# Kernel tuning notes

Hardware: AMD Instinct MI355X
Metric: run time of the kernel (lower is better)

The kernel has to match this reference:

```python
import jax, jax.numpy as jnp
import numpy as np
from jax import lax

# dims
B = 1024          # batch
C_IN = 8          # board feature planes
HW = 8            # board side
FN = 16           # filter_num
SEN, INT, OUT = 1024, 2048, 1024
TOT = SEN + INT + OUT            # 4096
CNN_OUT = sum((HW - k + 1) ** 2 for k in range(1, 9)) * FN  # 204*FN = 3264
NUM_OUT = 1968
LORA_R = 64
LORA_SCALE = 128.0 / LORA_R      # alpha / rank = 2.0
TIMESTEPS = 5
DENSITY = 0.3


def setup_inputs() -> dict:
    key = jax.random.key(0)
    ks = jax.random.split(key, 20)
    inp = {"x": jax.random.normal(ks[0], (B, HW, HW, C_IN), dtype=jnp.float32)}
    # conv bank: kernels 1..8, OIHW layout
    for i, k in enumerate(range(1, 9)):
        inp[f"conv_w{k}"] = jax.random.normal(ks[1 + i], (FN, C_IN, k, k), dtype=jnp.float32) * (1.0 / np.sqrt(C_IN * k * k))
    inp["conv_b"] = jnp.zeros((8, FN), dtype=jnp.float32)
    # recurrent weight with sparsity pattern (mask = W != 0, as in register_buffer('sparsity_mask', W_init != 0))
    Wd = jax.random.normal(ks[9], (TOT, TOT), dtype=jnp.float32) * 0.02
    mask = (jax.random.uniform(ks[10], (TOT, TOT)) < DENSITY).astype(jnp.float32)
    inp["W"] = Wd * mask
    inp["lora_A"] = jax.random.normal(ks[11], (TOT, LORA_R), dtype=jnp.float32) * 0.02
    inp["lora_B"] = jax.random.normal(ks[12], (LORA_R, TOT), dtype=jnp.float32) * 0.02
    inp["ip_w"] = jax.random.normal(ks[13], (CNN_OUT, SEN), dtype=jnp.float32) * (1.0 / np.sqrt(CNN_OUT))
    inp["ip_b"] = jnp.zeros((SEN,), dtype=jnp.float32)
    inp["out_w"] = jax.random.normal(ks[14], (OUT, NUM_OUT), dtype=jnp.float32) * (1.0 / np.sqrt(OUT))
    inp["out_b"] = jnp.zeros((NUM_OUT,), dtype=jnp.float32)
    return inp


def _forward(x, conv_w1, conv_w2, conv_w3, conv_w4, conv_w5, conv_w6, conv_w7, conv_w8,
             conv_b, W, lora_A, lora_B, ip_w, ip_b, out_w, out_b):
    xn = jnp.transpose(x, (0, 3, 1, 2))  # NHWC -> NCHW, as x.permute(0,3,1,2)
    feats = []
    for i, cw in enumerate([conv_w1, conv_w2, conv_w3, conv_w4, conv_w5, conv_w6, conv_w7, conv_w8]):
        y = lax.conv_general_dilated(xn, cw, (1, 1), 'VALID',
                                     dimension_numbers=('NCHW', 'OIHW', 'NCHW'))
        y = jax.nn.relu(y + conv_b[i][None, :, None, None])  # use_relu=True
        feats.append(y.reshape(y.shape[0], -1))
    feat = jnp.concatenate(feats, axis=1)  # [B, CNN_OUT]

    # effective W with LoRA + sparsity mask
    mask = (W != 0).astype(W.dtype)
    W_eff = (W + (lora_A @ lora_B) * LORA_SCALE) * mask

    E = feat @ ip_w + ip_b                           # input_proj (no dropout: drop_out=False)
    E_pad = jnp.pad(E, ((0, 0), (0, TOT - SEN)))     # E feeds only the sensory block

    # The nine block matmuls S@Wss + I@Wrs + O@Wos etc. equal slices of state @ W_eff.
    state = jnp.zeros((x.shape[0], TOT), dtype=W.dtype)
    for t in range(TIMESTEPS):
        nxt = state @ W_eff
        if t == 0:
            nxt = nxt + E_pad
        nxt = state + nxt          # use_residual=True
        state = jax.nn.relu(nxt)

    O_state = state[:, SEN + INT:]
    return O_state @ out_w + out_b


def reference(x, conv_w1, conv_w2, conv_w3, conv_w4, conv_w5, conv_w6, conv_w7, conv_w8,
              conv_b, W, lora_A, lora_B, ip_w, ip_b, out_w, out_b):
    return _forward(x, conv_w1, conv_w2, conv_w3, conv_w4, conv_w5, conv_w6, conv_w7, conv_w8,
                    conv_b, W, lora_A, lora_B, ip_w, ip_b, out_w, out_b)
```

## Files before the change

kernel.cpp:

```cpp
#include <hip/hip_runtime.h>
#include <stdint.h>

typedef unsigned short u16;
typedef __attribute__((ext_vector_type(8))) short bf16x8;
typedef __attribute__((ext_vector_type(4))) float f32x4;

__device__ __forceinline__ u16 f2bf(float f) {
  union { float f; uint32_t u; } v; v.f = f;
  uint32_t u = v.u;
  return (u16)((u + 0x7fffu + ((u >> 16) & 1u)) >> 16);
}

__device__ __forceinline__ void gl_lds16(const void* g, void* l) {
  __builtin_amdgcn_global_load_lds(
      (const __attribute__((address_space(1))) uint32_t*)g,
      (__attribute__((address_space(3))) uint32_t*)l, 16, 0, 0);
}

__constant__ int c_off[9] = {0, 1024, 1808, 2384, 2784, 3040, 3184, 3248, 3264};

__global__ __launch_bounds__(256)
void prep_all(const float* __restrict__ x, u16* __restrict__ Xb,
              const float* __restrict__ lA, u16* __restrict__ lAb,
              const float* __restrict__ ip_w, u16* __restrict__ ip_wt,
              const float* __restrict__ out_w, u16* __restrict__ out_wt,
              const float* __restrict__ lB, u16* __restrict__ lBt,
              const float* w1, const float* w2, const float* w3, const float* w4,
              const float* w5, const float* w6, const float* w7, const float* w8,
              const float* __restrict__ cb,
              u16* __restrict__ Wct, float* __restrict__ bias_c) {
  __shared__ float tile[64][65];
  int b = blockIdx.x;
  const int t = threadIdx.x;
  if (b < 512) {
    const int i = b * 256 + t;
    const float4 v = ((const float4*)x)[i];
    ((ushort4*)Xb)[i] = make_ushort4(f2bf(v.x), f2bf(v.y), f2bf(v.z), f2bf(v.w));
    return;
  }
  b -= 512;
  if (b < 256) {
    const int i = b * 256 + t;
    const float4 v = ((const float4*)lA)[i];
    ((ushort4*)lAb)[i] = make_ushort4(f2bf(v.x), f2bf(v.y), f2bf(v.z), f2bf(v.w));
    return;
  }
  b -= 256;
  if (b < 1392) {
    const float* src; u16* dst; int R, C, bx, by;
    if (b < 816)        { src = ip_w;  dst = ip_wt;  R = 3264; C = 1024; bx = b % 16; by = b / 16; }
    else if (b < 1328)  { b -= 816;  src = out_w; dst = out_wt; R = 1024; C = 1968; bx = b % 32; by = b / 32; }
    else                { b -= 1328; src = lB;    dst = lBt;    R = 64;   C = 4096; bx = b;      by = 0; }
    const int rb = by << 6, cbs = bx << 6;
    for (int i = 0; i < 16; ++i) {
      const int idx = t + (i << 8);
      const int r = idx >> 6, c = idx & 63;
      float v = 0.f;
      if (cbs + c < C) v = src[(size_t)(rb + r) * C + cbs + c];
      tile[r][c] = v;
    }
    __syncthreads();
    for (int i = 0; i < 16; ++i) {
      const int idx = t + (i << 8);
      const int c = idx >> 6, r = idx & 63;
      dst[(size_t)(cbs + c) * R + rb + r] = f2bf(tile[r][c]);
    }
    return;
  }
  const int o = b - 1392;
  u16* row = Wct + (size_t)o * 512;
  if (t < 128) *(ushort4*)(row + (t << 2)) = make_ushort4(0, 0, 0, 0);
  if (o >= 3264) {
    if (t == 0) bias_c[o] = 0.f;
    return;
  }
  __syncthreads();
  const float* ws[8] = {w1, w2, w3, w4, w5, w6, w7, w8};
  int kidx = 0;
  while (o >= c_off[kidx + 1]) ++kidx;
  const int ks = kidx + 1;
  const int s  = 8 - kidx;
  const int r  = o - c_off[kidx];
  const int f   = r / (s * s);
  const int rem = r - f * s * s;
  const int oi  = rem / s;
  const int oj  = rem - oi * s;
  const float* w = ws[kidx] + (size_t)f * 8 * ks * ks;
  const int ne = 8 * ks * ks;
  for (int e = t; e < ne; e += 256) {
    const int c  = e / (ks * ks);
    const int er = e - c * ks * ks;
    const int di = er / ks;
    const int dj = er - di * ks;
    row[((oi + di) * 8 + (oj + dj)) * 8 + c] = f2bf(w[(c * ks + di) * ks + dj]);
  }
  if (t == 0) bias_c[o] = cb[kidx * 16 + f];
}

__global__ __launch_bounds__(256)
void weff2(const float* __restrict__ W, const u16* __restrict__ lBt,
           const u16* __restrict__ lAb, u16* __restrict__ Wt) {
  __shared__ __align__(16) u16 As_[64 * 64];
  __shared__ __align__(16) u16 Bs_[64 * 64];
  __shared__ __align__(16) float Wl[64 * 64];
  __shared__ u16 Ct[64 * 68];
  const int t = threadIdx.x;
  const int w = t >> 6, lane = t & 63;
  const int nb = blockIdx.x << 6, kb = blockIdx.y << 6;
  const int m0 = (w & 1) << 5, n0 = (w >> 1) << 5;
  const int lr = lane & 15, lq = lane >> 4;

  for (int i = 0; i < 2; ++i) {
    const int c   = (w << 7) + (i << 6) + lane;
    const int row = c >> 3;
    const int kg  = (c & 7) ^ (row & 7);
    gl_lds16(lBt + (size_t)(nb + row) * 64 + (kg << 3), (char*)As_ + c * 16);
    gl_lds16(lAb + (size_t)(kb + row) * 64 + (kg << 3), (char*)Bs_ + c * 16);
  }
  for (int i = 0; i < 4; ++i) {
    const int c   = (w << 8) + (i << 6) + lane;
    const int row = c >> 4;
    const int cc  = (c & 15) ^ (row & 15);
    gl_lds16(W + (size_t)(kb + row) * 4096 + nb + (cc << 2), (char*)Wl + c * 16);
  }
  __syncthreads();

  f32x4 acc[2][2] = {};
  for (int kk = 0; kk < 2; ++kk) {
    const int kg = (kk << 2) + lq;
    const int sw = (kg ^ (lr & 7)) << 3;
    bf16x8 af[2], bf[2];
    for (int i = 0; i < 2; ++i)
      af[i] = *(const bf16x8*)&As_[(m0 + (i << 4) + lr) * 64 + sw];
    for (int j = 0; j < 2; ++j)
      bf[j] = *(const bf16x8*)&Bs_[(n0 + (j << 4) + lr) * 64 + sw];
    for (int i = 0; i < 2; ++i)
      for (int j = 0; j < 2; ++j)
        acc[i][j] = __builtin_amdgcn_mfma_f32_16x16x32_bf16(af[i], bf[j], acc[i][j], 0, 0, 0);
  }

  for (int i = 0; i < 2; ++i) {
    for (int j = 0; j < 2; ++j) {
      const int cg  = n0 + (j << 4) + lr;
      const int rg0 = m0 + (i << 4) + (lq << 2);
      const int ch  = (rg0 >> 2) ^ (cg & 15);
      const float4 wv4 = *(const float4*)&Wl[cg * 64 + (ch << 2)];
      const float wv[4] = {wv4.x, wv4.y, wv4.z, wv4.w};
      for (int r = 0; r < 4; ++r)
        Ct[(rg0 + r) * 68 + cg] =
            (wv[r] != 0.f) ? f2bf(wv[r] + 2.0f * acc[i][j][r]) : (u16)0;
    }
  }
  __syncthreads();

  const int row = t >> 2, kp = (t & 3) << 4;
  u16* dst = Wt + (size_t)(nb + row) * 4096 + kb + kp;
  const u16* src = &Ct[row * 68 + kp];
  for (int i = 0; i < 4; ++i)
    *(ushort4*)(dst + (i << 2)) = *(const ushort4*)(src + (i << 2));
}

template<int EPI>
__global__ __launch_bounds__(256)
void gemm128(const u16* __restrict__ A, int lda,
             const u16* __restrict__ Bt, int ldb, int K,
             const float* __restrict__ bias,
             const float* __restrict__ st_in, int st_ld,
             float* __restrict__ outf, int outf_ld,
             u16* __restrict__ outb, int outb_ld, int nvalid) {
  __shared__ __align__(16) u16 As[2][64 * 64];
  __shared__ __align__(16) u16 Bs[2][128 * 64];
  const int t = threadIdx.x;
  const int w = t >> 6, lane = t & 63;
  const int mb = blockIdx.y << 6, nb = blockIdx.x << 7;
  const int m0 = (w & 1) << 5, n0 = (w >> 1) << 6;
  const int lr = lane & 15, lq = lane >> 4;

  f32x4 acc[2][4] = {};
  const int nk = K >> 6;

  auto stage = [&](int kt, int buf) {
    const int kb = kt << 6;
    for (int i = 0; i < 2; ++i) {
      const int c   = (w << 7) + (i << 6) + lane;
      const int row = c >> 3;
      const int kg  = (c & 7) ^ (row & 7);
      gl_lds16(A + (size_t)(mb + row) * lda + kb + (kg << 3),
               (char*)As[buf] + c * 16);
    }
    for (int i = 0; i < 4; ++i) {
      const int c   = (w << 8) + (i << 6) + lane;
      const int row = c >> 3;
      const int kg  = (c & 7) ^ (row & 7);
      gl_lds16(Bt + (size_t)(nb + row) * ldb + kb + (kg << 3),
               (char*)Bs[buf] + c * 16);
    }
  };

  stage(0, 0);
  for (int kt = 0; kt < nk; ++kt) {
    const int buf = kt & 1;
    __syncthreads();
    if (kt + 1 < nk) stage(kt + 1, buf ^ 1);
    for (int kk = 0; kk < 2; ++kk) {
      const int kg = (kk << 2) + lq;
      const int sw = (kg ^ (lr & 7)) << 3;
      bf16x8 af[2], bf[4];
      for (int i = 0; i < 2; ++i)
        af[i] = *(const bf16x8*)&As[buf][(m0 + (i << 4) + lr) * 64 + sw];
      for (int j = 0; j < 4; ++j)
        bf[j] = *(const bf16x8*)&Bs[buf][(n0 + (j << 4) + lr) * 64 + sw];
      for (int i = 0; i < 2; ++i)
        for (int j = 0; j < 4; ++j)
          acc[i][j] = __builtin_amdgcn_mfma_f32_16x16x32_bf16(af[i], bf[j], acc[i][j], 0, 0, 0);
    }
  }

  for (int i = 0; i < 2; ++i) {
    for (int j = 0; j < 4; ++j) {
      const int cg = nb + n0 + (j << 4) + lr;
      for (int r = 0; r < 4; ++r) {
        const int rg = mb + m0 + (i << 4) + (lq << 2) + r;
        float v = acc[i][j][r];
        if (EPI == 1) {
          v += st_in[(size_t)rg * st_ld + cg];
          v = v > 0.f ? v : 0.f;
          outf[(size_t)rg * outf_ld + cg] = v;
          outb[(size_t)rg * outb_ld + cg] = f2bf(v);
        } else if (EPI == 2) {
          if (cg < nvalid)
            outf[(size_t)rg * outf_ld + cg] = v + bias[cg];
        } else {
          v += bias[cg];
          v = v > 0.f ? v : 0.f;
          outb[(size_t)rg * outb_ld + cg] = f2bf(v);
        }
      }
    }
  }
}

__global__ __launch_bounds__(256)
void gemm_e(const u16* __restrict__ A, const u16* __restrict__ Bt,
            float* __restrict__ part) {
  __shared__ __align__(16) u16 As[2][64 * 64];
  __shared__ __align__(16) u16 Bs[2][128 * 64];
  const int t = threadIdx.x;
  const int w = t >> 6, lane = t & 63;
  const int mb = blockIdx.y << 6, nb = blockIdx.x << 7;
  const int m0 = (w & 1) << 5, n0 = (w >> 1) << 6;
  const int lr = lane & 15, lq = lane >> 4;
  const int z = blockIdx.z;
  const int k0 = z * 832;
  const int nk = (z == 3) ? 12 : 13;

  f32x4 acc[2][4] = {};

  auto stage = [&](int kt, int buf) {
    const int kb = k0 + (kt << 6);
    for (int i = 0; i < 2; ++i) {
      const int c   = (w << 7) + (i << 6) + lane;
      const int row = c >> 3;
      const int kg  = (c & 7) ^ (row & 7);
      gl_lds16(A + (size_t)(mb + row) * 3328 + kb + (kg << 3),
               (char*)As[buf] + c * 16);
    }
    for (int i = 0; i < 4; ++i) {
      const int c   = (w << 8) + (i << 6) + lane;
      const int row = c >> 3;
      const int kg  = (c & 7) ^ (row & 7);
      gl_lds16(Bt + (size_t)(nb + row) * 3264 + kb + (kg << 3),
               (char*)Bs[buf] + c * 16);
    }
  };

  stage(0, 0);
  for (int kt = 0; kt < nk; ++kt) {
    const int buf = kt & 1;
    __syncthreads();
    if (kt + 1 < nk) stage(kt + 1, buf ^ 1);
    for (int kk = 0; kk < 2; ++kk) {
      const int kg = (kk << 2) + lq;
      const int sw = (kg ^ (lr & 7)) << 3;
      bf16x8 af[2], bf[4];
      for (int i = 0; i < 2; ++i)
        af[i] = *(const bf16x8*)&As[buf][(m0 + (i << 4) + lr) * 64 + sw];
      for (int j = 0; j < 4; ++j)
        bf[j] = *(const bf16x8*)&Bs[buf][(n0 + (j << 4) + lr) * 64 + sw];
      for (int i = 0; i < 2; ++i)
        for (int j = 0; j < 4; ++j)
          acc[i][j] = __builtin_amdgcn_mfma_f32_16x16x32_bf16(af[i], bf[j], acc[i][j], 0, 0, 0);
    }
  }

  float* dst = part + (size_t)z * 1024 * 1024;
  for (int i = 0; i < 2; ++i)
    for (int j = 0; j < 4; ++j) {
      const int cg = nb + n0 + (j << 4) + lr;
      for (int r = 0; r < 4; ++r) {
        const int rg = mb + m0 + (i << 4) + (lq << 2) + r;
        dst[(size_t)rg * 1024 + cg] = acc[i][j][r];
      }
    }
}

__global__ __launch_bounds__(256)
void e_combine(const float* __restrict__ part, const float* __restrict__ bias,
               float* __restrict__ st_f, u16* __restrict__ st_b) {
  const int i = (blockIdx.x * 256 + threadIdx.x) << 2;
  const int row = i >> 12, col = i & 4095;
  if (col < 1024) {
    const int pi = (row << 10) + col;
    const float4 a = *(const float4*)&part[pi];
    const float4 b = *(const float4*)&part[1024 * 1024 + pi];
    const float4 c = *(const float4*)&part[2 * 1024 * 1024 + pi];
    const float4 d = *(const float4*)&part[3 * 1024 * 1024 + pi];
    const float4 bs = *(const float4*)&bias[col];
    float v[4] = {a.x + b.x + c.x + d.x + bs.x, a.y + b.y + c.y + d.y + bs.y,
                  a.z + b.z + c.z + d.z + bs.z, a.w + b.w + c.w + d.w + bs.w};
    u16 o[4];
    for (int r = 0; r < 4; ++r) {
      v[r] = v[r] > 0.f ? v[r] : 0.f;
      o[r] = f2bf(v[r]);
    }
    *(float4*)&st_f[i] = make_float4(v[0], v[1], v[2], v[3]);
    *(ushort4*)&st_b[i] = make_ushort4(o[0], o[1], o[2], o[3]);
  } else {
    *(float4*)&st_f[i] = make_float4(0.f, 0.f, 0.f, 0.f);
    *(ushort4*)&st_b[i] = make_ushort4(0, 0, 0, 0);
  }
}

extern "C" void kernel_launch(void* const* d_in, const int* in_sizes, int n_in,
                              void* d_out, int out_size, void* d_ws, size_t ws_size,
                              hipStream_t stream) {
  const float* x     = (const float*)d_in[0];
  const float* cw[8];
  for (int i = 0; i < 8; ++i) cw[i] = (const float*)d_in[1 + i];
  const float* convb = (const float*)d_in[9];
  const float* W     = (const float*)d_in[10];
  const float* lA    = (const float*)d_in[11];
  const float* lB    = (const float*)d_in[12];
  const float* ip_w  = (const float*)d_in[13];
  const float* ip_b  = (const float*)d_in[14];
  const float* out_w = (const float*)d_in[15];
  const float* out_b = (const float*)d_in[16];
  float* out = (float*)d_out;

  char* p = (char*)d_ws;
  u16* feat   = (u16*)p;  p += (size_t)1024 * 3328 * 2;
  u16* ip_wt  = (u16*)p;  p += (size_t)1024 * 3264 * 2;
  u16* out_wt = (u16*)p;  p += (size_t)2048 * 1024 * 2;
  u16* Wt     = (u16*)p;  p += (size_t)4096 * 4096 * 2;
  float* st_f[2];
  st_f[0] = (float*)p;    p += (size_t)1024 * 4096 * 4;
  st_f[1] = (float*)p;    p += (size_t)1024 * 4096 * 4;
  u16* st_b[2];
  st_b[0] = (u16*)p;      p += (size_t)1024 * 4096 * 2;
  st_b[1] = (u16*)p;      p += (size_t)1024 * 4096 * 2;

  char* q = (char*)st_f[1];
  u16* Xb       = (u16*)q;  q += (size_t)1024 * 512 * 2;
  u16* Wct      = (u16*)q;  q += (size_t)3328 * 512 * 2;
  float* bias_c = (float*)q; q += (size_t)3328 * 4;
  u16* lBt      = (u16*)q;  q += (size_t)4096 * 64 * 2;
  u16* lAb      = (u16*)q;  q += (size_t)4096 * 64 * 2;
  float* Epart  = (float*)st_f[1];

  prep_all<<<5488, 256, 0, stream>>>(x, Xb, lA, lAb, ip_w, ip_wt,
                                     out_w, out_wt, lB, lBt,
                                     cw[0], cw[1], cw[2], cw[3],
                                     cw[4], cw[5], cw[6], cw[7], convb,
                                     Wct, bias_c);

  weff2<<<dim3(64, 64), 256, 0, stream>>>(W, lBt, lAb, Wt);

  gemm128<3><<<dim3(26, 16), 256, 0, stream>>>(Xb, 512, Wct, 512, 512,
      bias_c, nullptr, 0, nullptr, 0, feat, 3328, 3328);

  gemm_e<<<dim3(8, 16, 4), 256, 0, stream>>>(feat, ip_wt, Epart);
  e_combine<<<4096, 256, 0, stream>>>(Epart, ip_b, st_f[0], st_b[0]);

  gemm128<1><<<dim3(32, 16), 256, 0, stream>>>(st_b[0], 4096, Wt, 4096, 1024,
      nullptr, st_f[0], 4096, st_f[1], 4096, st_b[1], 4096, 4096);

  gemm128<1><<<dim3(32, 16), 256, 0, stream>>>(st_b[1], 4096, Wt, 4096, 4096,
      nullptr, st_f[1], 4096, st_f[0], 4096, st_b[0], 4096, 4096);
  gemm128<1><<<dim3(32, 16), 256, 0, stream>>>(st_b[0], 4096, Wt, 4096, 4096,
      nullptr, st_f[0], 4096, st_f[1], 4096, st_b[1], 4096, 4096);

  gemm128<1><<<dim3(8, 16), 256, 0, stream>>>(st_b[1], 4096,
      Wt + (size_t)3072 * 4096, 4096, 4096,
      nullptr, st_f[1] + 3072, 4096, st_f[0] + 3072, 4096,
      st_b[0] + 3072, 4096, 4096);

  gemm128<2><<<dim3(16, 16), 256, 0, stream>>>(st_b[0] + 3072, 4096, out_wt, 1024, 1024,
      out_b, nullptr, 0, out, 1968, nullptr, 0, 1968);
}
```

Baseline: 392.7 us.

## Use single-wave GEMM blocks with vmcnt-based double buffering, no barriers

The 256-thread, 4-wave GEMM kernels become 64-thread single-wave kernels that each compute a 64x64 (or 32x64) tile. Because one wave owns the whole block, __syncthreads is dropped. Two stages are prefetched, and completion of the async global-to-LDS loads is tracked with explicit s_waitcnt vmcnt/lgkmcnt counts. This removes barrier stalls and gives more blocks for scheduling, at the cost of lower per-block data reuse and LDS-sharing per wave, and correctness now relies on hand-counted outstanding loads.

After: 417.4 us. 6.3% more time.

```diff
diff --git a/kernel.cpp b/kernel.cpp
--- a/kernel.cpp
+++ b/kernel.cpp
@@ -160,36 +160,36 @@
     *(ushort4*)(dst + (i << 2)) = *(const ushort4*)(src + (i << 2));
 }
 
-template<int EPI>
-__global__ __launch_bounds__(256)
-void gemm128(const u16* __restrict__ A, int lda,
-             const u16* __restrict__ Bt, int ldb, int K,
-             const float* __restrict__ bias,
-             const float* __restrict__ st_in, int st_ld,
-             float* __restrict__ outf, int outf_ld,
-             u16* __restrict__ outb, int outb_ld, int nvalid) {
-  __shared__ __align__(16) u16 As[2][64 * 64];
-  __shared__ __align__(16) u16 Bs[2][128 * 64];
-  const int t = threadIdx.x;
-  const int w = t >> 6, lane = t & 63;
-  const int mb = blockIdx.y << 6, nb = blockIdx.x << 7;
-  const int m0 = (w & 1) << 5, n0 = (w >> 1) << 6;
+template<int EPI, int MF>
+__global__ __launch_bounds__(64)
+void gemm64(const u16* __restrict__ A, int lda,
+            const u16* __restrict__ Bt, int ldb, int K,
+            const float* __restrict__ bias,
+            const float* __restrict__ st_in, int st_ld,
+            float* __restrict__ outf, int outf_ld,
+            u16* __restrict__ outb, int outb_ld, int nvalid) {
+  __shared__ __align__(16) u16 As[2][MF * 16 * 64];
+  __shared__ __align__(16) u16 Bs[2][64 * 64];
+  const int lane = threadIdx.x;
+  const int mb = blockIdx.y * (MF * 16), nb = blockIdx.x << 6;
   const int lr = lane & 15, lq = lane >> 4;
 
-  f32x4 acc[2][4] = {};
+  f32x4 acc[MF][4] = {};
   const int nk = K >> 6;
 
   auto stage = [&](int kt, int buf) {
     const int kb = kt << 6;
-    for (int i = 0; i < 2; ++i) {
-      const int c   = (w << 7) + (i << 6) + lane;
+#pragma unroll
+    for (int i = 0; i < MF * 2; ++i) {
+      const int c   = (i << 6) + lane;
       const int row = c >> 3;
       const int kg  = (c & 7) ^ (row & 7);
       gl_lds16(A + (size_t)(mb + row) * lda + kb + (kg << 3),
                (char*)As[buf] + c * 16);
     }
-    for (int i = 0; i < 4; ++i) {
-      const int c   = (w << 8) + (i << 6) + lane;
+#pragma unroll
+    for (int i = 0; i < 8; ++i) {
+      const int c   = (i << 6) + lane;
       const int row = c >> 3;
       const int kg  = (c & 7) ^ (row & 7);
       gl_lds16(Bt + (size_t)(nb + row) * ldb + kb + (kg << 3),
@@ -198,29 +198,46 @@
   };
 
   stage(0, 0);
+  stage(1, 1);
   for (int kt = 0; kt < nk; ++kt) {
     const int buf = kt & 1;
-    __syncthreads();
-    if (kt + 1 < nk) stage(kt + 1, buf ^ 1);
+    if (kt + 1 < nk) {
+      if constexpr (MF == 4) asm volatile("s_waitcnt vmcnt(16)" ::: "memory");
+      else                   asm volatile("s_waitcnt vmcnt(12)" ::: "memory");
+    } else {
+      asm volatile("s_waitcnt vmcnt(0)" ::: "memory");
+    }
+#pragma unroll
     for (int kk = 0; kk < 2; ++kk) {
       const int kg = (kk << 2) + lq;
       const int sw = (kg ^ (lr & 7)) << 3;
-      bf16x8 af[2], bf[4];
-      for (int i = 0; i < 2; ++i)
-        af[i] = *(const bf16x8*)&As[buf][(m0 + (i << 4) + lr) * 64 + sw];
+      bf16x8 af[MF], bf[4];
+#pragma unroll
+      for (int i = 0; i < MF; ++i)
+        af[i] = *(const bf16x8*)&As[buf][((i << 4) + lr) * 64 + sw];
+#pragma unroll
       for (int j = 0; j < 4; ++j)
-        bf[j] = *(const bf16x8*)&Bs[buf][(n0 + (j << 4) + lr) * 64 + sw];
-      for (int i = 0; i < 2; ++i)
+        bf[j] = *(const bf16x8*)&Bs[buf][((j << 4) + lr) * 64 + sw];
+#pragma unroll
+      for (int i = 0; i < MF; ++i)
+#pragma unroll
         for (int j = 0; j < 4; ++j)
           acc[i][j] = __builtin_amdgcn_mfma_f32_16x16x32_bf16(af[i], bf[j], acc[i][j], 0, 0, 0);
     }
-  }
-
-  for (int i = 0; i < 2; ++i) {
+    if (kt + 2 < nk) {
+      asm volatile("s_waitcnt lgkmcnt(0)" ::: "memory");
+      stage(kt + 2, buf);
+    }
+  }
+
+#pragma unroll
+  for (int i = 0; i < MF; ++i) {
+#pragma unroll
     for (int j = 0; j < 4; ++j) {
-      const int cg = nb + n0 + (j << 4) + lr;
+      const int cg = nb + (j << 4) + lr;
+#pragma unroll
       for (int r = 0; r < 4; ++r) {
-        const int rg = mb + m0 + (i << 4) + (lq << 2) + r;
+        const int rg = mb + (i << 4) + (lq << 2) + r;
         float v = acc[i][j][r];
         if (EPI == 1) {
           v += st_in[(size_t)rg * st_ld + cg];
@@ -240,33 +257,33 @@
   }
 }
 
-__global__ __launch_bounds__(256)
-void gemm_e(const u16* __restrict__ A, const u16* __restrict__ Bt,
-            float* __restrict__ part) {
+__global__ __launch_bounds__(64)
+void gemm_e64(const u16* __restrict__ A, const u16* __restrict__ Bt,
+              float* __restrict__ part) {
   __shared__ __align__(16) u16 As[2][64 * 64];
-  __shared__ __align__(16) u16 Bs[2][128 * 64];
-  const int t = threadIdx.x;
-  const int w = t >> 6, lane = t & 63;
-  const int mb = blockIdx.y << 6, nb = blockIdx.x << 7;
-  const int m0 = (w & 1) << 5, n0 = (w >> 1) << 6;
+  __shared__ __align__(16) u16 Bs[2][64 * 64];
+  const int lane = threadIdx.x;
+  const int mb = blockIdx.y << 6, nb = blockIdx.x << 6;
   const int lr = lane & 15, lq = lane >> 4;
   const int z = blockIdx.z;
   const int k0 = z * 832;
   const int nk = (z == 3) ? 12 : 13;
 
-  f32x4 acc[2][4] = {};
+  f32x4 acc[4][4] = {};
 
   auto stage = [&](int kt, int buf) {
     const int kb = k0 + (kt << 6);
-    for (int i = 0; i < 2; ++i) {
-      const int c   = (w << 7) + (i << 6) + lane;
+#pragma unroll
+    for (int i = 0; i < 8; ++i) {
+      const int c   = (i << 6) + lane;
       const int row = c >> 3;
       const int kg  = (c & 7) ^ (row & 7);
       gl_lds16(A + (size_t)(mb + row) * 3328 + kb + (kg << 3),
                (char*)As[buf] + c * 16);
     }
-    for (int i = 0; i < 4; ++i) {
-      const int c   = (w << 8) + (i << 6) + lane;
+#pragma unroll
+    for (int i = 0; i < 8; ++i) {
+      const int c   = (i << 6) + lane;
       const int row = c >> 3;
       const int kg  = (c & 7) ^ (row & 7);
       gl_lds16(Bt + (size_t)(nb + row) * 3264 + kb + (kg << 3),
@@ -275,30 +292,43 @@
   };
 
   stage(0, 0);
+  stage(1, 1);
   for (int kt = 0; kt < nk; ++kt) {
     const int buf = kt & 1;
-    __syncthreads();
-    if (kt + 1 < nk) stage(kt + 1, buf ^ 1);
+    if (kt + 1 < nk) asm volatile("s_waitcnt vmcnt(16)" ::: "memory");
+    else             asm volatile("s_waitcnt vmcnt(0)" ::: "memory");
+#pragma unroll
     for (int kk = 0; kk < 2; ++kk) {
       const int kg = (kk << 2) + lq;
       const int sw = (kg ^ (lr & 7)) << 3;
-      bf16x8 af[2], bf[4];
-      for (int i = 0; i < 2; ++i)
-        af[i] = *(const bf16x8*)&As[buf][(m0 + (i << 4) + lr) * 64 + sw];
+      bf16x8 af[4], bf[4];
+#pragma unroll
+      for (int i = 0; i < 4; ++i)
+        af[i] = *(const bf16x8*)&As[buf][((i << 4) + lr) * 64 + sw];
+#pragma unroll
       for (int j = 0; j < 4; ++j)
-        bf[j] = *(const bf16x8*)&Bs[buf][(n0 + (j << 4) + lr) * 64 + sw];
-      for (int i = 0; i < 2; ++i)
+        bf[j] = *(const bf16x8*)&Bs[buf][((j << 4) + lr) * 64 + sw];
+#pragma unroll
+      for (int i = 0; i < 4; ++i)
+#pragma unroll
         for (int j = 0; j < 4; ++j)
           acc[i][j] = __builtin_amdgcn_mfma_f32_16x16x32_bf16(af[i], bf[j], acc[i][j], 0, 0, 0);
     }
+    if (kt + 2 < nk) {
+      asm volatile("s_waitcnt lgkmcnt(0)" ::: "memory");
+      stage(kt + 2, buf);
+    }
   }
 
   float* dst = part + (size_t)z * 1024 * 1024;
-  for (int i = 0; i < 2; ++i)
+#pragma unroll
+  for (int i = 0; i < 4; ++i)
+#pragma unroll
     for (int j = 0; j < 4; ++j) {
-      const int cg = nb + n0 + (j << 4) + lr;
+      const int cg = nb + (j << 4) + lr;
+#pragma unroll
       for (int r = 0; r < 4; ++r) {
-        const int rg = mb + m0 + (i << 4) + (lq << 2) + r;
+        const int rg = mb + (i << 4) + (lq << 2) + r;
         dst[(size_t)rg * 1024 + cg] = acc[i][j][r];
       }
     }
@@ -375,25 +405,25 @@
 
   weff2<<<dim3(64, 64), 256, 0, stream>>>(W, lBt, lAb, Wt);
 
-  gemm128<3><<<dim3(26, 16), 256, 0, stream>>>(Xb, 512, Wct, 512, 512,
+  gemm64<3, 4><<<dim3(52, 16), 64, 0, stream>>>(Xb, 512, Wct, 512, 512,
       bias_c, nullptr, 0, nullptr, 0, feat, 3328, 3328);
 
-  gemm_e<<<dim3(8, 16, 4), 256, 0, stream>>>(feat, ip_wt, Epart);
+  gemm_e64<<<dim3(16, 16, 4), 64, 0, stream>>>(feat, ip_wt, Epart);
   e_combine<<<4096, 256, 0, stream>>>(Epart, ip_b, st_f[0], st_b[0]);
 
-  gemm128<1><<<dim3(32, 16), 256, 0, stream>>>(st_b[0], 4096, Wt, 4096, 1024,
+  gemm64<1, 4><<<dim3(64, 16), 64, 0, stream>>>(st_b[0], 4096, Wt, 4096, 1024,
       nullptr, st_f[0], 4096, st_f[1], 4096, st_b[1], 4096, 4096);
 
-  gemm128<1><<<dim3(32, 16), 256, 0, stream>>>(st_b[1], 4096, Wt, 4096, 4096,
+  gemm64<1, 4><<<dim3(64, 16), 64, 0, stream>>>(st_b[1], 4096, Wt, 4096, 4096,
       nullptr, st_f[1], 4096, st_f[0], 4096, st_b[0], 4096, 4096);
-  gemm128<1><<<dim3(32, 16), 256, 0, stream>>>(st_b[0], 4096, Wt, 4096, 4096,
+  gemm64<1, 4><<<dim3(64, 16), 64, 0, stream>>>(st_b[0], 4096, Wt, 4096, 4096,
       nullptr, st_f[0], 4096, st_f[1], 4096, st_b[1], 4096, 4096);
 
-  gemm128<1><<<dim3(8, 16), 256, 0, stream>>>(st_b[1], 4096,
+  gemm64<1, 2><<<dim3(16, 32), 64, 0, stream>>>(st_b[1], 4096,
       Wt + (size_t)3072 * 4096, 4096, 4096,
       nullptr, st_f[1] + 3072, 4096, st_f[0] + 3072, 4096,
       st_b[0] + 3072, 4096, 4096);
 
-  gemm128<2><<<dim3(16, 16), 256, 0, stream>>>(st_b[0] + 3072, 4096, out_wt, 1024, 1024,
+  gemm64<2, 2><<<dim3(32, 32), 64, 0, stream>>>(st_b[0] + 3072, 4096, out_wt, 1024, 1024,
       out_b, nullptr, 0, out, 1968, nullptr, 0, 1968);
 }
```

## Triple-buffer GEMM k-loop with explicit vmcnt waits and narrower tiles for small GEMMs

Applied to the files above, without the earlier changes.

Replaces the double-buffered GEMM k-loop with a three-stage LDS ring that prefetches two tiles ahead. It swaps __syncthreads for explicit s_waitcnt vmcnt plus s_barrier and raises wave priority around the MFMA block. The block N width is now a template parameter, so the last recurrent step and the output projection use 64-wide tiles and launch twice as many blocks to fill more CUs. The extra LDS stage cuts occupancy, and the hand-set vmcnt counts must match the number of loads issued per stage.

Result: no change. 393.6 us (+0.2%).

```diff
diff --git a/kernel.cpp b/kernel.cpp
--- a/kernel.cpp
+++ b/kernel.cpp
@@ -160,27 +160,29 @@
     *(ushort4*)(dst + (i << 2)) = *(const ushort4*)(src + (i << 2));
 }
 
-template<int EPI>
+template<int EPI, int NR>
 __global__ __launch_bounds__(256)
-void gemm128(const u16* __restrict__ A, int lda,
-             const u16* __restrict__ Bt, int ldb, int K,
-             const float* __restrict__ bias,
-             const float* __restrict__ st_in, int st_ld,
-             float* __restrict__ outf, int outf_ld,
-             u16* __restrict__ outb, int outb_ld, int nvalid) {
-  __shared__ __align__(16) u16 As[2][64 * 64];
-  __shared__ __align__(16) u16 Bs[2][128 * 64];
+void gemm3b(const u16* __restrict__ A, int lda,
+            const u16* __restrict__ Bt, int ldb, int K,
+            const float* __restrict__ bias,
+            const float* __restrict__ st_in, int st_ld,
+            float* __restrict__ outf, int outf_ld,
+            u16* __restrict__ outb, int outb_ld, int nvalid) {
+  constexpr int BN = NR * 32;
+  __shared__ __align__(16) u16 As[3][64 * 64];
+  __shared__ __align__(16) u16 Bs[3][BN * 64];
   const int t = threadIdx.x;
   const int w = t >> 6, lane = t & 63;
-  const int mb = blockIdx.y << 6, nb = blockIdx.x << 7;
-  const int m0 = (w & 1) << 5, n0 = (w >> 1) << 6;
+  const int mb = blockIdx.y << 6, nb = blockIdx.x * BN;
+  const int m0 = (w & 1) << 5, n0 = (w >> 1) * (NR << 4);
   const int lr = lane & 15, lq = lane >> 4;
 
-  f32x4 acc[2][4] = {};
+  f32x4 acc[2][NR] = {};
   const int nk = K >> 6;
 
   auto stage = [&](int kt, int buf) {
     const int kb = kt << 6;
+#pragma unroll
     for (int i = 0; i < 2; ++i) {
       const int c   = (w << 7) + (i << 6) + lane;
       const int row = c >> 3;
@@ -188,8 +190,9 @@
       gl_lds16(A + (size_t)(mb + row) * lda + kb + (kg << 3),
                (char*)As[buf] + c * 16);
     }
-    for (int i = 0; i < 4; ++i) {
-      const int c   = (w << 8) + (i << 6) + lane;
+#pragma unroll
+    for (int i = 0; i < NR; ++i) {
+      const int c   = w * (NR * 64) + (i << 6) + lane;
       const int row = c >> 3;
       const int kg  = (c & 7) ^ (row & 7);
       gl_lds16(Bt + (size_t)(nb + row) * ldb + kb + (kg << 3),
@@ -198,27 +201,46 @@
   };
 
   stage(0, 0);
+  stage(1, 1);
   for (int kt = 0; kt < nk; ++kt) {
-    const int buf = kt & 1;
-    __syncthreads();
-    if (kt + 1 < nk) stage(kt + 1, buf ^ 1);
+    const int buf = kt % 3;
+    if (kt + 1 < nk) {
+      if constexpr (NR == 4) asm volatile("s_waitcnt vmcnt(6)" ::: "memory");
+      else                   asm volatile("s_waitcnt vmcnt(4)" ::: "memory");
+    } else {
+      asm volatile("s_waitcnt vmcnt(0)" ::: "memory");
+    }
+    __builtin_amdgcn_s_barrier();
+    asm volatile("" ::: "memory");
+    __builtin_amdgcn_sched_barrier(0);
+    if (kt + 2 < nk) stage(kt + 2, (kt + 2) % 3);
+    __builtin_amdgcn_s_setprio(1);
+#pragma unroll
     for (int kk = 0; kk < 2; ++kk) {
       const int kg = (kk << 2) + lq;
       const int sw = (kg ^ (lr & 7)) << 3;
-      bf16x8 af[2], bf[4];
+      bf16x8 af[2], bf[NR];
+#pragma unroll
       for (int i = 0; i < 2; ++i)
         af[i] = *(const bf16x8*)&As[buf][(m0 + (i << 4) + lr) * 64 + sw];
-      for (int j = 0; j < 4; ++j)
+#pragma unroll
+      for (int j = 0; j < NR; ++j)
         bf[j] = *(const bf16x8*)&Bs[buf][(n0 + (j << 4) + lr) * 64 + sw];
+#pragma unroll
       for (int i = 0; i < 2; ++i)
-        for (int j = 0; j < 4; ++j)
+#pragma unroll
+        for (int j = 0; j < NR; ++j)
           acc[i][j] = __builtin_amdgcn_mfma_f32_16x16x32_bf16(af[i], bf[j], acc[i][j], 0, 0, 0);
     }
-  }
-
+    __builtin_amdgcn_s_setprio(0);
+  }
+
+#pragma unroll
   for (int i = 0; i < 2; ++i) {
-    for (int j = 0; j < 4; ++j) {
+#pragma unroll
+    for (int j = 0; j < NR; ++j) {
       const int cg = nb + n0 + (j << 4) + lr;
+#pragma unroll
       for (int r = 0; r < 4; ++r) {
         const int rg = mb + m0 + (i << 4) + (lq << 2) + r;
         float v = acc[i][j][r];
@@ -241,10 +263,10 @@
 }
 
 __global__ __launch_bounds__(256)
-void gemm_e(const u16* __restrict__ A, const u16* __restrict__ Bt,
-            float* __restrict__ part) {
-  __shared__ __align__(16) u16 As[2][64 * 64];
-  __shared__ __align__(16) u16 Bs[2][128 * 64];
+void gemm_e3b(const u16* __restrict__ A, const u16* __restrict__ Bt,
+              float* __restrict__ part) {
+  __shared__ __align__(16) u16 As[3][64 * 64];
+  __shared__ __align__(16) u16 Bs[3][128 * 64];
   const int t = threadIdx.x;
   const int w = t >> 6, lane = t & 63;
   const int mb = blockIdx.y << 6, nb = blockIdx.x << 7;
@@ -258,6 +280,7 @@
 
   auto stage = [&](int kt, int buf) {
     const int kb = k0 + (kt << 6);
+#pragma unroll
     for (int i = 0; i < 2; ++i) {
       const int c   = (w << 7) + (i << 6) + lane;
       const int row = c >> 3;
@@ -265,6 +288,7 @@
       gl_lds16(A + (size_t)(mb + row) * 3328 + kb + (kg << 3),
                (char*)As[buf] + c * 16);
     }
+#pragma unroll
     for (int i = 0; i < 4; ++i) {
       const int c   = (w << 8) + (i << 6) + lane;
       const int row = c >> 3;
@@ -275,28 +299,43 @@
   };
 
   stage(0, 0);
+  stage(1, 1);
   for (int kt = 0; kt < nk; ++kt) {
-    const int buf = kt & 1;
-    __syncthreads();
-    if (kt + 1 < nk) stage(kt + 1, buf ^ 1);
+    const int buf = kt % 3;
+    if (kt + 1 < nk) asm volatile("s_waitcnt vmcnt(6)" ::: "memory");
+    else             asm volatile("s_waitcnt vmcnt(0)" ::: "memory");
+    __builtin_amdgcn_s_barrier();
+    asm volatile("" ::: "memory");
+    __builtin_amdgcn_sched_barrier(0);
+    if (kt + 2 < nk) stage(kt + 2, (kt + 2) % 3);
+    __builtin_amdgcn_s_setprio(1);
+#pragma unroll
     for (int kk = 0; kk < 2; ++kk) {
       const int kg = (kk << 2) + lq;
       const int sw = (kg ^ (lr & 7)) << 3;
       bf16x8 af[2], bf[4];
+#pragma unroll
       for (int i = 0; i < 2; ++i)
         af[i] = *(const bf16x8*)&As[buf][(m0 + (i << 4) + lr) * 64 + sw];
+#pragma unroll
       for (int j = 0; j < 4; ++j)
         bf[j] = *(const bf16x8*)&Bs[buf][(n0 + (j << 4) + lr) * 64 + sw];
+#pragma unroll
       for (int i = 0; i < 2; ++i)
+#pragma unroll
         for (int j = 0; j < 4; ++j)
           acc[i][j] = __builtin_amdgcn_mfma_f32_16x16x32_bf16(af[i], bf[j], acc[i][j], 0, 0, 0);
     }
+    __builtin_amdgcn_s_setprio(0);
   }
 
   float* dst = part + (size_t)z * 1024 * 1024;
+#pragma unroll
   for (int i = 0; i < 2; ++i)
+#pragma unroll
     for (int j = 0; j < 4; ++j) {
       const int cg = nb + n0 + (j << 4) + lr;
+#pragma unroll
       for (int r = 0; r < 4; ++r) {
         const int rg = mb + m0 + (i << 4) + (lq << 2) + r;
         dst[(size_t)rg * 1024 + cg] = acc[i][j][r];
@@ -375,25 +414,25 @@
 
   weff2<<<dim3(64, 64), 256, 0, stream>>>(W, lBt, lAb, Wt);
 
-  gemm128<3><<<dim3(26, 16), 256, 0, stream>>>(Xb, 512, Wct, 512, 512,
+  gemm3b<3, 4><<<dim3(26, 16), 256, 0, stream>>>(Xb, 512, Wct, 512, 512,
       bias_c, nullptr, 0, nullptr, 0, feat, 3328, 3328);
 
-  gemm_e<<<dim3(8, 16, 4), 256, 0, stream>>>(feat, ip_wt, Epart);
+  gemm_e3b<<<dim3(8, 16, 4), 256, 0, stream>>>(feat, ip_wt, Epart);
   e_combine<<<4096, 256, 0, stream>>>(Epart, ip_b, st_f[0], st_b[0]);
 
-  gemm128<1><<<dim3(32, 16), 256, 0, stream>>>(st_b[0], 4096, Wt, 4096, 1024,
+  gemm3b<1, 4><<<dim3(32, 16), 256, 0, stream>>>(st_b[0], 4096, Wt, 4096, 1024,
       nullptr, st_f[0], 4096, st_f[1], 4096, st_b[1], 4096, 4096);
 
-  gemm128<1><<<dim3(32, 16), 256, 0, stream>>>(st_b[1], 4096, Wt, 4096, 4096,
+  gemm3b<1, 4><<<dim3(32, 16), 256, 0, stream>>>(st_b[1], 4096, Wt, 4096, 4096,
       nullptr, st_f[1], 4096, st_f[0], 4096, st_b[0], 4096, 4096);
-  gemm128<1><<<dim3(32, 16), 256, 0, stream>>>(st_b[0], 4096, Wt, 4096, 4096,
+  gemm3b<1, 4><<<dim3(32, 16), 256, 0, stream>>>(st_b[0], 4096, Wt, 4096, 4096,
       nullptr, st_f[0], 4096, st_f[1], 4096, st_b[1], 4096, 4096);
 
-  gemm128<1><<<dim3(8, 16), 256, 0, stream>>>(st_b[1], 4096,
+  gemm3b<1, 2><<<dim3(16, 16), 256, 0, stream>>>(st_b[1], 4096,
       Wt + (size_t)3072 * 4096, 4096, 4096,
       nullptr, st_f[1] + 3072, 4096, st_f[0] + 3072, 4096,
       st_b[0] + 3072, 4096, 4096);
 
-  gemm128<2><<<dim3(16, 16), 256, 0, stream>>>(st_b[0] + 3072, 4096, out_wt, 1024, 1024,
+  gemm3b<2, 2><<<dim3(32, 16), 256, 0, stream>>>(st_b[0] + 3072, 4096, out_wt, 1024, 1024,
       out_b, nullptr, 0, out, 1968, nullptr, 0, 1968);
 }
```

## Fuse conv GEMM into W_eff kernel, split-K last step, narrower output tiles

Applied to the files above, without the earlier changes.

Merges the conv-bank GEMM and the W_eff construction into one launch so the small conv GEMM overlaps the larger LoRA/mask kernel. The final recurrent step, which only needs output columns 3072+, moves from a 128-block GEMM to a 4-way split-K GEMM with a combine kernel, which raises occupancy. The third step skips the fp32 state write for columns it no longer needs. The output GEMM uses 64-wide N tiles for more blocks, and the prep transpose writes vectorized columns. The cost is extra partial-sum traffic and one more launch.

Result: faster. 347.3 us (-11.6%).

```diff
diff --git a/kernel.cpp b/kernel.cpp
--- a/kernel.cpp
+++ b/kernel.cpp
@@ -60,10 +60,13 @@
       tile[r][c] = v;
     }
     __syncthreads();
-    for (int i = 0; i < 16; ++i) {
-      const int idx = t + (i << 8);
-      const int c = idx >> 6, r = idx & 63;
-      dst[(size_t)(cbs + c) * R + rb + r] = f2bf(tile[r][c]);
+    const int c = t & 63, q = t >> 6;
+    u16* dcol = dst + (size_t)(cbs + c) * R + rb;
+    for (int v4 = 0; v4 < 4; ++v4) {
+      const int r0 = (q << 4) + (v4 << 2);
+      *(ushort4*)(dcol + r0) = make_ushort4(
+          f2bf(tile[r0][c]), f2bf(tile[r0 + 1][c]),
+          f2bf(tile[r0 + 2][c]), f2bf(tile[r0 + 3][c]));
     }
     return;
   }
@@ -97,16 +100,135 @@
   if (t == 0) bias_c[o] = cb[kidx * 16 + f];
 }
 
-__global__ __launch_bounds__(256)
-void weff2(const float* __restrict__ W, const u16* __restrict__ lBt,
-           const u16* __restrict__ lAb, u16* __restrict__ Wt) {
-  __shared__ __align__(16) u16 As_[64 * 64];
-  __shared__ __align__(16) u16 Bs_[64 * 64];
-  __shared__ __align__(16) float Wl[64 * 64];
-  __shared__ u16 Ct[64 * 68];
+template<int EPI, int NR>
+__device__ __forceinline__
+void gemm_body(char* lds,
+               const u16* __restrict__ A, int lda,
+               const u16* __restrict__ Bt, int ldb, int K,
+               const float* __restrict__ bias,
+               const float* __restrict__ st_in, int st_ld,
+               float* __restrict__ outf, int outf_ld,
+               u16* __restrict__ outb, int outb_ld, int nvalid,
+               int mb, int nb, int stf_c0) {
+  constexpr int BN = NR * 32;
+  u16 (*As)[64 * 64] = reinterpret_cast<u16 (*)[64 * 64]>(lds);
+  u16 (*Bs)[BN * 64] = reinterpret_cast<u16 (*)[BN * 64]>(lds + 2 * 64 * 64 * 2);
   const int t = threadIdx.x;
   const int w = t >> 6, lane = t & 63;
-  const int nb = blockIdx.x << 6, kb = blockIdx.y << 6;
+  const int m0 = (w & 1) << 5, n0 = (w >> 1) * (NR << 4);
+  const int lr = lane & 15, lq = lane >> 4;
+
+  f32x4 acc[2][NR] = {};
+  const int nk = K >> 6;
+
+  auto stage = [&](int kt, int buf) {
+    const int kb = kt << 6;
+#pragma unroll
+    for (int i = 0; i < 2; ++i) {
+      const int c   = (w << 7) + (i << 6) + lane;
+      const int row = c >> 3;
+      const int kg  = (c & 7) ^ (row & 7);
+      gl_lds16(A + (size_t)(mb + row) * lda + kb + (kg << 3),
+               (char*)As[buf] + c * 16);
+    }
+#pragma unroll
+    for (int i = 0; i < NR; ++i) {
+      const int c   = w * (NR * 64) + (i << 6) + lane;
+      const int row = c >> 3;
+      const int kg  = (c & 7) ^ (row & 7);
+      gl_lds16(Bt + (size_t)(nb + row) * ldb + kb + (kg << 3),
+               (char*)Bs[buf] + c * 16);
+    }
+  };
+
+  stage(0, 0);
+  for (int kt = 0; kt < nk; ++kt) {
+    const int buf = kt & 1;
+    __syncthreads();
+    if (kt + 1 < nk) stage(kt + 1, buf ^ 1);
+#pragma unroll
+    for (int kk = 0; kk < 2; ++kk) {
+      const int kg = (kk << 2) + lq;
+      const int sw = (kg ^ (lr & 7)) << 3;
+      bf16x8 af[2], bf[NR];
+#pragma unroll
+      for (int i = 0; i < 2; ++i)
+        af[i] = *(const bf16x8*)&As[buf][(m0 + (i << 4) + lr) * 64 + sw];
+#pragma unroll
+      for (int j = 0; j < NR; ++j)
+        bf[j] = *(const bf16x8*)&Bs[buf][(n0 + (j << 4) + lr) * 64 + sw];
+#pragma unroll
+      for (int i = 0; i < 2; ++i)
+#pragma unroll
+        for (int j = 0; j < NR; ++j)
+          acc[i][j] = __builtin_amdgcn_mfma_f32_16x16x32_bf16(af[i], bf[j], acc[i][j], 0, 0, 0);
+    }
+  }
+
+#pragma unroll
+  for (int i = 0; i < 2; ++i) {
+#pragma unroll
+    for (int j = 0; j < NR; ++j) {
+      const int cg = nb + n0 + (j << 4) + lr;
+#pragma unroll
+      for (int r = 0; r < 4; ++r) {
+        const int rg = mb + m0 + (i << 4) + (lq << 2) + r;
+        float v = acc[i][j][r];
+        if (EPI == 0) {
+          outf[(size_t)rg * outf_ld + cg] = v;
+        } else if (EPI == 1) {
+          v += st_in[(size_t)rg * st_ld + cg];
+          v = v > 0.f ? v : 0.f;
+          if (cg >= stf_c0) outf[(size_t)rg * outf_ld + cg] = v;
+          outb[(size_t)rg * outb_ld + cg] = f2bf(v);
+        } else if (EPI == 2) {
+          if (cg < nvalid)
+            outf[(size_t)rg * outf_ld + cg] = v + bias[cg];
+        } else {
+          v += bias[cg];
+          v = v > 0.f ? v : 0.f;
+          outb[(size_t)rg * outb_ld + cg] = f2bf(v);
+        }
+      }
+    }
+  }
+}
+
+template<int EPI, int NR>
+__global__ __launch_bounds__(256)
+void gemm128(const u16* __restrict__ A, int lda,
+             const u16* __restrict__ Bt, int ldb, int K,
+             const float* __restrict__ bias,
+             const float* __restrict__ st_in, int st_ld,
+             float* __restrict__ outf, int outf_ld,
+             u16* __restrict__ outb, int outb_ld, int nvalid, int stf_c0) {
+  __shared__ __align__(16) char lds[2 * 64 * 64 * 2 + 2 * NR * 32 * 64 * 2];
+  gemm_body<EPI, NR>(lds, A, lda, Bt, ldb, K, bias, st_in, st_ld,
+                     outf, outf_ld, outb, outb_ld, nvalid,
+                     blockIdx.y << 6, blockIdx.x * (NR * 32), stf_c0);
+}
+
+__global__ __launch_bounds__(256)
+void weff_conv(const float* __restrict__ W, const u16* __restrict__ lBt,
+               const u16* __restrict__ lAb, u16* __restrict__ Wt,
+               const u16* __restrict__ Xb, const u16* __restrict__ Wct,
+               const float* __restrict__ bias_c, u16* __restrict__ feat) {
+  __shared__ __align__(16) char lds[49152];
+  const int b = blockIdx.x;
+  const int t = threadIdx.x;
+  if (b < 416) {
+    const int bx = b % 26, by = b / 26;
+    gemm_body<3, 4>(lds, Xb, 512, Wct, 512, 512, bias_c, nullptr, 0,
+                    nullptr, 0, feat, 3328, 3328, by << 6, bx << 7, 0);
+    return;
+  }
+  u16*   As_ = (u16*)lds;
+  u16*   Bs_ = (u16*)(lds + 8192);
+  float* Wl  = (float*)(lds + 16384);
+  u16*   Ct  = (u16*)(lds + 32768);
+  const int b2 = b - 416;
+  const int w = t >> 6, lane = t & 63;
+  const int nb = (b2 & 63) << 6, kb = (b2 >> 6) << 6;
   const int m0 = (w & 1) << 5, n0 = (w >> 1) << 5;
   const int lr = lane & 15, lq = lane >> 4;
 
@@ -160,148 +282,26 @@
     *(ushort4*)(dst + (i << 2)) = *(const ushort4*)(src + (i << 2));
 }
 
-template<int EPI>
-__global__ __launch_bounds__(256)
-void gemm128(const u16* __restrict__ A, int lda,
-             const u16* __restrict__ Bt, int ldb, int K,
-             const float* __restrict__ bias,
-             const float* __restrict__ st_in, int st_ld,
-             float* __restrict__ outf, int outf_ld,
-             u16* __restrict__ outb, int outb_ld, int nvalid) {
-  __shared__ __align__(16) u16 As[2][64 * 64];
-  __shared__ __align__(16) u16 Bs[2][128 * 64];
-  const int t = threadIdx.x;
-  const int w = t >> 6, lane = t & 63;
-  const int mb = blockIdx.y << 6, nb = blockIdx.x << 7;
-  const int m0 = (w & 1) << 5, n0 = (w >> 1) << 6;
-  const int lr = lane & 15, lq = lane >> 4;
-
-  f32x4 acc[2][4] = {};
-  const int nk = K >> 6;
-
-  auto stage = [&](int kt, int buf) {
-    const int kb = kt << 6;
-    for (int i = 0; i < 2; ++i) {
-      const int c   = (w << 7) + (i << 6) + lane;
-      const int row = c >> 3;
-      const int kg  = (c & 7) ^ (row & 7);
-      gl_lds16(A + (size_t)(mb + row) * lda + kb + (kg << 3),
-               (char*)As[buf] + c * 16);
-    }
-    for (int i = 0; i < 4; ++i) {
-      const int c   = (w << 8) + (i << 6) + lane;
-      const int row = c >> 3;
-      const int kg  = (c & 7) ^ (row & 7);
-      gl_lds16(Bt + (size_t)(nb + row) * ldb + kb + (kg << 3),
-               (char*)Bs[buf] + c * 16);
-    }
-  };
-
-  stage(0, 0);
-  for (int kt = 0; kt < nk; ++kt) {
-    const int buf = kt & 1;
-    __syncthreads();
-    if (kt + 1 < nk) stage(kt + 1, buf ^ 1);
-    for (int kk = 0; kk < 2; ++kk) {
-      const int kg = (kk << 2) + lq;
-      const int sw = (kg ^ (lr & 7)) << 3;
-      bf16x8 af[2], bf[4];
-      for (int i = 0; i < 2; ++i)
-        af[i] = *(const bf16x8*)&As[buf][(m0 + (i << 4) + lr) * 64 + sw];
-      for (int j = 0; j < 4; ++j)
-        bf[j] = *(const bf16x8*)&Bs[buf][(n0 + (j << 4) + lr) * 64 + sw];
-      for (int i = 0; i < 2; ++i)
-        for (int j = 0; j < 4; ++j)
-          acc[i][j] = __builtin_amdgcn_mfma_f32_16x16x32_bf16(af[i], bf[j], acc[i][j], 0, 0, 0);
-    }
-  }
-
-  for (int i = 0; i < 2; ++i) {
-    for (int j = 0; j < 4; ++j) {
-      const int cg = nb + n0 + (j << 4) + lr;
-      for (int r = 0; r < 4; ++r) {
-        const int rg = mb + m0 + (i << 4) + (lq << 2) + r;
-        float v = acc[i][j][r];
-        if (EPI == 1) {
-          v += st_in[(size_t)rg * st_ld + cg];
-          v = v > 0.f ? v : 0.f;
-          outf[(size_t)rg * outf_ld + cg] = v;
-          outb[(size_t)rg * outb_ld + cg] = f2bf(v);
-        } else if (EPI == 2) {
-          if (cg < nvalid)
-            outf[(size_t)rg * outf_ld + cg] = v + bias[cg];
-        } else {
-          v += bias[cg];
-          v = v > 0.f ? v : 0.f;
-          outb[(size_t)rg * outb_ld + cg] = f2bf(v);
-        }
-      }
-    }
-  }
-}
-
 __global__ __launch_bounds__(256)
 void gemm_e(const u16* __restrict__ A, const u16* __restrict__ Bt,
             float* __restrict__ part) {
-  __shared__ __align__(16) u16 As[2][64 * 64];
-  __shared__ __align__(16) u16 Bs[2][128 * 64];
-  const int t = threadIdx.x;
-  const int w = t >> 6, lane = t & 63;
-  const int mb = blockIdx.y << 6, nb = blockIdx.x << 7;
-  const int m0 = (w & 1) << 5, n0 = (w >> 1) << 6;
-  const int lr = lane & 15, lq = lane >> 4;
+  __shared__ __align__(16) char lds[49152];
   const int z = blockIdx.z;
   const int k0 = z * 832;
   const int nk = (z == 3) ? 12 : 13;
-
-  f32x4 acc[2][4] = {};
-
-  auto stage = [&](int kt, int buf) {
-    const int kb = k0 + (kt << 6);
-    for (int i = 0; i < 2; ++i) {
-      const int c   = (w << 7) + (i << 6) + lane;
-      const int row = c >> 3;
-      const int kg  = (c & 7) ^ (row & 7);
-      gl_lds16(A + (size_t)(mb + row) * 3328 + kb + (kg << 3),
-               (char*)As[buf] + c * 16);
-    }
-    for (int i = 0; i < 4; ++i) {
-      const int c   = (w << 8) + (i << 6) + lane;
-      const int row = c >> 3;
-      const int kg  = (c & 7) ^ (row & 7);
-      gl_lds16(Bt + (size_t)(nb + row) * 3264 + kb + (kg << 3),
-               (char*)Bs[buf] + c * 16);
-    }
-  };
-
-  stage(0, 0);
-  for (int kt = 0; kt < nk; ++kt) {
-    const int buf = kt & 1;
-    __syncthreads();
-    if (kt + 1 < nk) stage(kt + 1, buf ^ 1);
-    for (int kk = 0; kk < 2; ++kk) {
-      const int kg = (kk << 2) + lq;
-      const int sw = (kg ^ (lr & 7)) << 3;
-      bf16x8 af[2], bf[4];
-      for (int i = 0; i < 2; ++i)
-        af[i] = *(const bf16x8*)&As[buf][(m0 + (i << 4) + lr) * 64 + sw];
-      for (int j = 0; j < 4; ++j)
-        bf[j] = *(const bf16x8*)&Bs[buf][(n0 + (j << 4) + lr) * 64 + sw];
-      for (int i = 0; i < 2; ++i)
-        for (int j = 0; j < 4; ++j)
-          acc[i][j] = __builtin_amdgcn_mfma_f32_16x16x32_bf16(af[i], bf[j], acc[i][j], 0, 0, 0);
-    }
-  }
-
-  float* dst = part + (size_t)z * 1024 * 1024;
-  for (int i = 0; i < 2; ++i)
-    for (int j = 0; j < 4; ++j) {
-      const int cg = nb + n0 + (j << 4) + lr;
-      for (int r = 0; r < 4; ++r) {
-        const int rg = mb + m0 + (i << 4) + (lq << 2) + r;
-        dst[(size_t)rg * 1024 + cg] = acc[i][j][r];
-      }
-    }
+  gemm_body<0, 4>(lds, A + k0, 3328, Bt + k0, 3264, nk << 6,
+                  nullptr, nullptr, 0, part + ((size_t)z << 20), 1024,
+                  nullptr, 0, 0, blockIdx.y << 6, blockIdx.x << 7, 0);
+}
+
+__global__ __launch_bounds__(256)
+void gemm_p4(const u16* __restrict__ A, const u16* __restrict__ Bt,
+             float* __restrict__ part) {
+  __shared__ __align__(16) char lds[32768];
+  const int z = blockIdx.z;
+  gemm_body<0, 2>(lds, A + (z << 10), 4096, Bt + (z << 10), 4096, 1024,
+                  nullptr, nullptr, 0, part + ((size_t)z << 20), 1024,
+                  nullptr, 0, 0, blockIdx.y << 6, blockIdx.x << 6, 0);
 }
 
 __global__ __launch_bounds__(256)
@@ -331,6 +331,26 @@
   }
 }
 
+__global__ __launch_bounds__(256)
+void t4_combine(const float* __restrict__ part, const float* __restrict__ st_in,
+                u16* __restrict__ st_b) {
+  const int i = (blockIdx.x * 256 + threadIdx.x) << 2;
+  const int r = i >> 10, c = i & 1023;
+  const float4 a  = *(const float4*)&part[i];
+  const float4 b  = *(const float4*)&part[(1 << 20) + i];
+  const float4 cc = *(const float4*)&part[(2 << 20) + i];
+  const float4 d  = *(const float4*)&part[(3 << 20) + i];
+  const float4 s  = *(const float4*)&st_in[(size_t)r * 4096 + 3072 + c];
+  float v[4] = {a.x + b.x + cc.x + d.x + s.x, a.y + b.y + cc.y + d.y + s.y,
+                a.z + b.z + cc.z + d.z + s.z, a.w + b.w + cc.w + d.w + s.w};
+  u16 o[4];
+  for (int k = 0; k < 4; ++k) {
+    v[k] = v[k] > 0.f ? v[k] : 0.f;
+    o[k] = f2bf(v[k]);
+  }
+  *(ushort4*)&st_b[(size_t)r * 4096 + 3072 + c] = make_ushort4(o[0], o[1], o[2], o[3]);
+}
+
 extern "C" void kernel_launch(void* const* d_in, const int* in_sizes, int n_in,
                               void* d_out, int out_size, void* d_ws, size_t ws_size,
                               hipStream_t stream) {
@@ -366,6 +386,7 @@
   u16* lBt      = (u16*)q;  q += (size_t)4096 * 64 * 2;
   u16* lAb      = (u16*)q;  q += (size_t)4096 * 64 * 2;
   float* Epart  = (float*)st_f[1];
+  float* Tpart  = (float*)st_f[0];
 
   prep_all<<<5488, 256, 0, stream>>>(x, Xb, lA, lAb, ip_w, ip_wt,
                                      out_w, out_wt, lB, lBt,
@@ -373,27 +394,23 @@
                                      cw[4], cw[5], cw[6], cw[7], convb,
                                      Wct, bias_c);
 
-  weff2<<<dim3(64, 64), 256, 0, stream>>>(W, lBt, lAb, Wt);
-
-  gemm128<3><<<dim3(26, 16), 256, 0, stream>>>(Xb, 512, Wct, 512, 512,
-      bias_c, nullptr, 0, nullptr, 0, feat, 3328, 3328);
+  weff_conv<<<4512, 256, 0, stream>>>(W, lBt, lAb, Wt, Xb, Wct, bias_c, feat);
 
   gemm_e<<<dim3(8, 16, 4), 256, 0, stream>>>(feat, ip_wt, Epart);
   e_combine<<<4096, 256, 0, stream>>>(Epart, ip_b, st_f[0], st_b[0]);
 
-  gemm128<1><<<dim3(32, 16), 256, 0, stream>>>(st_b[0], 4096, Wt, 4096, 1024,
-      nullptr, st_f[0], 4096, st_f[1], 4096, st_b[1], 4096, 4096);
-
-  gemm128<1><<<dim3(32, 16), 256, 0, stream>>>(st_b[1], 4096, Wt, 4096, 4096,
-      nullptr, st_f[1], 4096, st_f[0], 4096, st_b[0], 4096, 4096);
-  gemm128<1><<<dim3(32, 16), 256, 0, stream>>>(st_b[0], 4096, Wt, 4096, 4096,
-      nullptr, st_f[0], 4096, st_f[1], 4096, st_b[1], 4096, 4096);
-
-  gemm128<1><<<dim3(8, 16), 256, 0, stream>>>(st_b[1], 4096,
-      Wt + (size_t)3072 * 4096, 4096, 4096,
-      nullptr, st_f[1] + 3072, 4096, st_f[0] + 3072, 4096,
-      st_b[0] + 3072, 4096, 4096);
-
-  gemm128<2><<<dim3(16, 16), 256, 0, stream>>>(st_b[0] + 3072, 4096, out_wt, 1024, 1024,
-      out_b, nullptr, 0, out, 1968, nullptr, 0, 1968);
-}
+  gemm128<1, 4><<<dim3(32, 16), 256, 0, stream>>>(st_b[0], 4096, Wt, 4096, 1024,
+      nullptr, st_f[0], 4096, st_f[1], 4096, st_b[1], 4096, 4096, 0);
+
+  gemm128<1, 4><<<dim3(32, 16), 256, 0, stream>>>(st_b[1], 4096, Wt, 4096, 4096,
+      nullptr, st_f[1], 4096, st_f[0], 4096, st_b[0], 4096, 4096, 0);
+  gemm128<1, 4><<<dim3(32, 16), 256, 0, stream>>>(st_b[0], 4096, Wt, 4096, 4096,
+      nullptr, st_f[0], 4096, st_f[1], 4096, st_b[1], 4096, 4096, 3072);
+
+  gemm_p4<<<dim3(16, 16, 4), 256, 0, stream>>>(st_b[1],
+      Wt + (size_t)3072 * 4096, Tpart);
+  t4_combine<<<1024, 256, 0, stream>>>(Tpart, st_f[1], st_b[0]);
+
+  gemm128<2, 2><<<dim3(32, 16), 256, 0, stream>>>(st_b[0] + 3072, 4096, out_wt, 1024, 1024,
+      out_b, nullptr, 0, out, 1968, nullptr, 0, 1968, 0);
+}
```
